# Kernel tuning notes

Measured on AMD Instinct MI355X. Metric: run time of the kernel, lower is better.

Reference implementation:

```python
import jax, jax.numpy as jnp
import numpy as np

NUM_CLASSES = 100
NUM_PROTOS = 10
FEAT_DIM = 1024
BATCH = 16384
NALL = NUM_CLASSES * NUM_PROTOS


def setup_inputs() -> dict:
    key = jax.random.key(0)
    k1, k2, k3 = jax.random.split(key, 3)
    x = jax.random.normal(k1, (BATCH, FEAT_DIM), dtype=jnp.float32)
    protos = jax.random.normal(k2, (NALL, FEAT_DIM), dtype=jnp.float32)
    enc_w = jax.random.normal(k3, (FEAT_DIM, FEAT_DIM), dtype=jnp.float32) / np.sqrt(FEAT_DIM)
    enc_b = jnp.zeros((FEAT_DIM,), dtype=jnp.float32)
    return {"x": x, "protos": protos, "enc_w": enc_w, "enc_b": enc_b}


def reference(x, protos, enc_w, enc_b):
    # encoder(protos): linear projection, (nall, F)
    ep = protos @ enc_w + enc_b
    # Pairwise euclidean distance via GEMM-based squared-distance trick:
    x_sq = jnp.sum(x * x, axis=-1, keepdims=True)            # (B, 1)
    p_sq = jnp.sum(ep * ep, axis=-1)                          # (nall,)
    d2 = x_sq - 2.0 * (x @ ep.T) + p_sq[None, :]              # (B, nall)
    d = jnp.sqrt(jnp.maximum(d2, 0.0))                        # L2 norm, clamp fp error
    # reshape matches torch: index = proto * num_classes + class
    d = d.reshape(x.shape[0], NUM_PROTOS, NUM_CLASSES)
    return jnp.min(d, axis=1)                                 # (B, num_classes)
```

## Files before the change

kernel.cpp:

```cpp
#include <hip/hip_runtime.h>
#include <hip/hip_bf16.h>
#include <stdint.h>

#define FEAT 1024
#define NALL 1000
#define NCLS 100

typedef __attribute__((ext_vector_type(8))) short short8;
typedef __attribute__((ext_vector_type(4))) float f32x4;
typedef __attribute__((ext_vector_type(4))) unsigned short us4;

__device__ __forceinline__ unsigned short f2bf(float f) {
    union { float f; uint32_t u; } v; v.f = f;
    uint32_t u = v.u;
    return (unsigned short)((u + 0x7FFFu + ((u >> 16) & 1u)) >> 16);
}

__device__ __forceinline__ void gload16(const void* g, void* l) {
    __builtin_amdgcn_global_load_lds((__attribute__((address_space(1))) void*)g,
                                     (__attribute__((address_space(3))) void*)l,
                                     16, 0, 0);
}

__global__ __launch_bounds__(256) void k_prep_all(const float* __restrict__ x,
                                                  unsigned short* __restrict__ xb,
                                                  float* __restrict__ xsq,
                                                  const float* __restrict__ p,
                                                  unsigned short* __restrict__ pb,
                                                  const float* __restrict__ w,
                                                  unsigned short* __restrict__ wt) {
    __shared__ float tile[32][33];
    int b = blockIdx.x;
    if (b < 4096) {
        int row = b * 4 + (threadIdx.x >> 6);
        int lane = threadIdx.x & 63;
        const float4* xr = (const float4*)(x + (size_t)row * FEAT);
        float s = 0.f;
#pragma unroll
        for (int i = 0; i < 4; ++i) {
            float4 v = xr[lane + i * 64];
            s += v.x * v.x + v.y * v.y + v.z * v.z + v.w * v.w;
            us4 o;
            o[0] = f2bf(v.x); o[1] = f2bf(v.y); o[2] = f2bf(v.z); o[3] = f2bf(v.w);
            *(us4*)(xb + (size_t)row * FEAT + (size_t)(lane + i * 64) * 4) = o;
        }
#pragma unroll
        for (int off = 32; off; off >>= 1) s += __shfl_xor(s, off);
        if (lane == 0) xsq[row] = s;
    } else if (b < 5120) {
        int row = b - 4096, t = threadIdx.x;
        us4 o;
        if (row < NALL) {
            float4 v = ((const float4*)(p + (size_t)row * FEAT))[t];
            o[0] = f2bf(v.x); o[1] = f2bf(v.y); o[2] = f2bf(v.z); o[3] = f2bf(v.w);
        } else {
            o[0] = 0; o[1] = 0; o[2] = 0; o[3] = 0;
        }
        *(us4*)(pb + (size_t)row * FEAT + (size_t)t * 4) = o;
    } else {
        int bb = b - 5120;
        int bx = bb & 31, by = bb >> 5;
        int tx = threadIdx.x & 31, ty = threadIdx.x >> 5;
#pragma unroll
        for (int i = 0; i < 4; ++i) {
            int r = by * 32 + ty + i * 8;
            tile[ty + i * 8][tx] = w[(size_t)r * FEAT + bx * 32 + tx];
        }
        __syncthreads();
#pragma unroll
        for (int i = 0; i < 4; ++i) {
            int r = bx * 32 + ty + i * 8;
            wt[(size_t)r * FEAT + by * 32 + tx] = f2bf(tile[tx][ty + i * 8]);
        }
    }
}

__global__ __launch_bounds__(256) void k_enc_gemm(const unsigned short* __restrict__ A,
                                                  const unsigned short* __restrict__ B,
                                                  const float* __restrict__ bias,
                                                  unsigned short* __restrict__ epb,
                                                  float* __restrict__ psq) {
    __shared__ __align__(16) char smem[16384];
    int bm0 = (blockIdx.x >> 4) * 64;
    int bn0 = (blockIdx.x & 15) * 64;
    int tid = threadIdx.x, lane = tid & 63, wid = tid >> 6;
    int wm = wid >> 1, wn = wid & 1;
    int ls = lane >> 4, lf = lane & 15;
    f32x4 acc[2][2] = {};
    for (int k0 = 0; k0 < FEAT; k0 += 64) {
        __syncthreads();
#pragma unroll
        for (int i = 0; i < 2; ++i) {
            int ci = wid + i * 4;
            int r = ci * 8 + (lane >> 3), c = (lane & 7) * 8;
            gload16(A + (size_t)(bm0 + r) * FEAT + k0 + c, smem + ci * 1024);
            gload16(B + (size_t)(bn0 + r) * FEAT + k0 + c, smem + 8192 + ci * 1024);
        }
        __syncthreads();
#pragma unroll
        for (int kk = 0; kk < 64; kk += 32) {
            short8 a[2], b[2];
#pragma unroll
            for (int f = 0; f < 2; ++f) {
                a[f] = *(const short8*)(smem + (wm * 32 + f * 16 + lf) * 128 + (kk + ls * 8) * 2);
                b[f] = *(const short8*)(smem + 8192 + (wn * 32 + f * 16 + lf) * 128 + (kk + ls * 8) * 2);
            }
#pragma unroll
            for (int fm = 0; fm < 2; ++fm)
#pragma unroll
                for (int fn = 0; fn < 2; ++fn)
                    acc[fm][fn] = __builtin_amdgcn_mfma_f32_16x16x32_bf16(a[fm], b[fn], acc[fm][fn], 0, 0, 0);
        }
    }
    int tr = ls * 4, tc = lf;
    float sq[2][4] = {};
#pragma unroll
    for (int fn = 0; fn < 2; ++fn) {
        int col = bn0 + wn * 32 + fn * 16 + tc;
        float bb = bias[col];
#pragma unroll
        for (int fm = 0; fm < 2; ++fm) {
#pragma unroll
            for (int r = 0; r < 4; ++r) {
                int row = bm0 + wm * 32 + fm * 16 + tr + r;
                if (row < NALL) {
                    unsigned short us = f2bf(acc[fm][fn][r] + bb);
                    union { uint32_t u; float f; } c; c.u = ((uint32_t)us) << 16;
                    sq[fm][r] += c.f * c.f;
                    int pr = (row % 100) * 10 + row / 100;
                    epb[(size_t)pr * FEAT + col] = us;
                }
            }
        }
    }
#pragma unroll
    for (int fm = 0; fm < 2; ++fm)
#pragma unroll
        for (int r = 0; r < 4; ++r) {
            float s = sq[fm][r];
            s += __shfl_xor(s, 1); s += __shfl_xor(s, 2);
            s += __shfl_xor(s, 4); s += __shfl_xor(s, 8);
            int row = bm0 + wm * 32 + fm * 16 + tr + r;
            if (lf == 0 && row < NALL) {
                int pr = (row % 100) * 10 + row / 100;
                atomicAdd(psq + pr, s);
            }
        }
}

__global__ __launch_bounds__(256, 4) void k_main(const unsigned short* __restrict__ xb,
                                                 const unsigned short* __restrict__ epb,
                                                 const float* __restrict__ xsq,
                                                 const float* __restrict__ psq,
                                                 float* __restrict__ out) {
    __shared__ __align__(16) char smem[27648];
    const int bid = blockIdx.x;
    const int swz = (bid & 7) * 208 + (bid >> 3);
    const int bm0 = (swz / 13) * 128;
    const int nt  = swz % 13;
    const int bn0 = (nt < 12) ? nt * 80 : 920;
    const int cls0 = (nt < 12) ? nt * 8 : 92;
    const int tid = threadIdx.x, lane = tid & 63, wid = tid >> 6;
    const int ls = lane >> 4, lf = lane & 15;
    float* xsq_s = (float*)(smem + 26624);
    float* psq_s = (float*)(smem + 27136);
    if (tid < 128) xsq_s[tid] = xsq[bm0 + tid];
    if (tid < 80)  psq_s[tid] = psq[bn0 + tid];

    const int sr = lane >> 3, scb = lane & 7;
    const int scol = ((scb ^ sr) << 3);
    const unsigned short* aptr[4];
    const unsigned short* bptr[3];
#pragma unroll
    for (int i = 0; i < 4; ++i)
        aptr[i] = xb + (size_t)(bm0 + (wid + i * 4) * 8 + sr) * FEAT + scol;
#pragma unroll
    for (int j = 0; j < 3; ++j) {
        int cj = wid + j * 4;
        bptr[j] = epb + (size_t)(bn0 + (cj < 10 ? cj : 0) * 8 + sr) * FEAT + scol;
    }

    int raA[2], raB[5];
#pragma unroll
    for (int f = 0; f < 2; ++f) raA[f] = (wid * 32 + f * 16 + lf) * 128;
#pragma unroll
    for (int f = 0; f < 5; ++f) raB[f] = 16384 + (f * 16 + lf) * 128;
    const int sw = lf & 7;

    f32x4 acc[2][5] = {};

    for (int t = 0; t < 16; ++t) {
        __syncthreads();
#pragma unroll
        for (int i = 0; i < 4; ++i)
            gload16(aptr[i], smem + (wid + i * 4) * 1024);
#pragma unroll
        for (int j = 0; j < 3; ++j) {
            int cj = wid + j * 4;
            if (cj < 10) gload16(bptr[j], smem + 16384 + cj * 1024);
        }
#pragma unroll
        for (int i = 0; i < 4; ++i) aptr[i] += 64;
#pragma unroll
        for (int j = 0; j < 3; ++j) bptr[j] += 64;
        __syncthreads();
#pragma unroll
        for (int kk2 = 0; kk2 < 2; ++kk2) {
            const int off = (((kk2 * 4 + ls) ^ sw) << 4);
            short8 a[2], b[5];
#pragma unroll
            for (int f = 0; f < 2; ++f)
                a[f] = *(const short8*)(smem + raA[f] + off);
#pragma unroll
            for (int f = 0; f < 5; ++f)
                b[f] = *(const short8*)(smem + raB[f] + off);
#pragma unroll
            for (int fm = 0; fm < 2; ++fm)
#pragma unroll
                for (int fn = 0; fn < 5; ++fn)
                    acc[fm][fn] = __builtin_amdgcn_mfma_f32_16x16x32_bf16(a[fm], b[fn], acc[fm][fn], 0, 0, 0);
        }
    }

    float* dls = (float*)smem;
    const int tr = ls * 4;
#pragma unroll
    for (int p = 0; p < 2; ++p) {
        __syncthreads();
#pragma unroll
        for (int fn = 0; fn < 5; ++fn) {
            int col = fn * 16 + lf;
            float pq = psq_s[col];
#pragma unroll
            for (int r = 0; r < 4; ++r) {
                float d2 = xsq_s[wid * 32 + p * 16 + tr + r] - 2.f * acc[p][fn][r] + pq;
                dls[(wid * 16 + tr + r) * 81 + col] = sqrtf(fmaxf(d2, 0.f));
            }
        }
        __syncthreads();
#pragma unroll
        for (int i = 0; i < 2; ++i) {
            int task = tid + i * 256;
            int rr = task >> 3, cl = task & 7;
            float m = 1e30f;
#pragma unroll
            for (int j = 0; j < 10; ++j) m = fminf(m, dls[rr * 81 + cl * 10 + j]);
            int grow = bm0 + (rr >> 4) * 32 + p * 16 + (rr & 15);
            out[(size_t)grow * NCLS + cls0 + cl] = m;
        }
    }
}

extern "C" void kernel_launch(void* const* d_in, const int* in_sizes, int n_in,
                              void* d_out, int out_size, void* d_ws, size_t ws_size,
                              hipStream_t stream) {
    const float* x      = (const float*)d_in[0];
    const float* protos = (const float*)d_in[1];
    const float* enc_w  = (const float*)d_in[2];
    const float* enc_b  = (const float*)d_in[3];
    float* out = (float*)d_out;
    char* ws = (char*)d_ws;

    unsigned short* xb  = (unsigned short*)ws;
    unsigned short* epb = (unsigned short*)(ws + 33554432);
    unsigned short* prb = (unsigned short*)(ws + 35651584);
    unsigned short* wtb = (unsigned short*)(ws + 37748736);
    float* xsq = (float*)(ws + 39845888);
    float* psq = (float*)(ws + 39911424);

    hipMemsetAsync(psq, 0, (size_t)NALL * 4, stream);

    k_prep_all<<<6144, 256, 0, stream>>>(x, xb, xsq, protos, prb, enc_w, wtb);
    k_enc_gemm<<<256, 256, 0, stream>>>(prb, wtb, enc_b, epb, psq);
    k_main<<<1664, 256, 0, stream>>>(xb, epb, xsq, psq, out);
}
```

Before: 99.29 us.

## Load A fragments directly to registers and double-buffer B tiles in LDS

Each wave now reads its A (x) MFMA fragments straight from global memory into registers, prefetching the next k-step while the current one computes. The B (prototype) tiles are double-buffered in LDS so the next tile's global_load_lds overlaps with the MFMA work, which leaves one barrier per iteration instead of two. Shared memory shrinks and the occupancy hint of 4 blocks is dropped from launch bounds. The risks are higher register pressure from the prefetch registers and less coalesced A loads, each lane fetching 16B pieces from a different row.

```diff
diff --git a/kernel.cpp b/kernel.cpp
--- a/kernel.cpp
+++ b/kernel.cpp
@@ -148,12 +148,12 @@
         }
 }
 
-__global__ __launch_bounds__(256, 4) void k_main(const unsigned short* __restrict__ xb,
-                                                 const unsigned short* __restrict__ epb,
-                                                 const float* __restrict__ xsq,
-                                                 const float* __restrict__ psq,
-                                                 float* __restrict__ out) {
-    __shared__ __align__(16) char smem[27648];
+__global__ __launch_bounds__(256) void k_main(const unsigned short* __restrict__ xb,
+                                              const unsigned short* __restrict__ epb,
+                                              const float* __restrict__ xsq,
+                                              const float* __restrict__ psq,
+                                              float* __restrict__ out) {
+    __shared__ __align__(16) char smem[22016];
     const int bid = blockIdx.x;
     const int swz = (bid & 7) * 208 + (bid >> 3);
     const int bm0 = (swz / 13) * 128;
@@ -162,64 +162,80 @@
     const int cls0 = (nt < 12) ? nt * 8 : 92;
     const int tid = threadIdx.x, lane = tid & 63, wid = tid >> 6;
     const int ls = lane >> 4, lf = lane & 15;
-    float* xsq_s = (float*)(smem + 26624);
-    float* psq_s = (float*)(smem + 27136);
+    float* xsq_s = (float*)(smem + 20992);
+    float* psq_s = (float*)(smem + 21504);
     if (tid < 128) xsq_s[tid] = xsq[bm0 + tid];
     if (tid < 80)  psq_s[tid] = psq[bn0 + tid];
 
+    const unsigned short* ga[2];
+#pragma unroll
+    for (int f = 0; f < 2; ++f)
+        ga[f] = xb + (size_t)(bm0 + wid * 32 + f * 16 + lf) * FEAT + ls * 8;
+
     const int sr = lane >> 3, scb = lane & 7;
     const int scol = ((scb ^ sr) << 3);
-    const unsigned short* aptr[4];
     const unsigned short* bptr[3];
-#pragma unroll
-    for (int i = 0; i < 4; ++i)
-        aptr[i] = xb + (size_t)(bm0 + (wid + i * 4) * 8 + sr) * FEAT + scol;
 #pragma unroll
     for (int j = 0; j < 3; ++j) {
         int cj = wid + j * 4;
         bptr[j] = epb + (size_t)(bn0 + (cj < 10 ? cj : 0) * 8 + sr) * FEAT + scol;
     }
 
-    int raA[2], raB[5];
-#pragma unroll
-    for (int f = 0; f < 2; ++f) raA[f] = (wid * 32 + f * 16 + lf) * 128;
-#pragma unroll
-    for (int f = 0; f < 5; ++f) raB[f] = 16384 + (f * 16 + lf) * 128;
+    int raB[5];
+#pragma unroll
+    for (int f = 0; f < 5; ++f) raB[f] = (f * 16 + lf) * 128;
     const int sw = lf & 7;
 
     f32x4 acc[2][5] = {};
-
+    short8 aC[2][2], aN[2][2];
+
+#pragma unroll
+    for (int f = 0; f < 2; ++f)
+#pragma unroll
+        for (int k2 = 0; k2 < 2; ++k2)
+            aC[f][k2] = *(const short8*)(ga[f] + k2 * 32);
+#pragma unroll
+    for (int j = 0; j < 3; ++j) {
+        int cj = wid + j * 4;
+        if (cj < 10) gload16(bptr[j], smem + cj * 1024);
+    }
+    __syncthreads();
+
+#pragma unroll
     for (int t = 0; t < 16; ++t) {
-        __syncthreads();
-#pragma unroll
-        for (int i = 0; i < 4; ++i)
-            gload16(aptr[i], smem + (wid + i * 4) * 1024);
-#pragma unroll
-        for (int j = 0; j < 3; ++j) {
-            int cj = wid + j * 4;
-            if (cj < 10) gload16(bptr[j], smem + 16384 + cj * 1024);
-        }
-#pragma unroll
-        for (int i = 0; i < 4; ++i) aptr[i] += 64;
-#pragma unroll
-        for (int j = 0; j < 3; ++j) bptr[j] += 64;
-        __syncthreads();
-#pragma unroll
-        for (int kk2 = 0; kk2 < 2; ++kk2) {
-            const int off = (((kk2 * 4 + ls) ^ sw) << 4);
-            short8 a[2], b[5];
+        const char* base = (const char*)smem + (t & 1) * 10240;
+        if (t < 15) {
 #pragma unroll
             for (int f = 0; f < 2; ++f)
-                a[f] = *(const short8*)(smem + raA[f] + off);
+#pragma unroll
+                for (int k2 = 0; k2 < 2; ++k2)
+                    aN[f][k2] = *(const short8*)(ga[f] + (t + 1) * 64 + k2 * 32);
+            char* nb = (char*)smem + ((t + 1) & 1) * 10240;
+#pragma unroll
+            for (int j = 0; j < 3; ++j) {
+                int cj = wid + j * 4;
+                if (cj < 10) gload16(bptr[j] + (t + 1) * 64, nb + cj * 1024);
+            }
+        }
+#pragma unroll
+        for (int k2 = 0; k2 < 2; ++k2) {
+            const int off = (((k2 * 4 + ls) ^ sw) << 4);
+            short8 b[5];
 #pragma unroll
             for (int f = 0; f < 5; ++f)
-                b[f] = *(const short8*)(smem + raB[f] + off);
+                b[f] = *(const short8*)(base + raB[f] + off);
 #pragma unroll
             for (int fm = 0; fm < 2; ++fm)
 #pragma unroll
                 for (int fn = 0; fn < 5; ++fn)
-                    acc[fm][fn] = __builtin_amdgcn_mfma_f32_16x16x32_bf16(a[fm], b[fn], acc[fm][fn], 0, 0, 0);
-        }
+                    acc[fm][fn] = __builtin_amdgcn_mfma_f32_16x16x32_bf16(aC[fm][k2], b[fn], acc[fm][fn], 0, 0, 0);
+        }
+        __syncthreads();
+#pragma unroll
+        for (int f = 0; f < 2; ++f)
+#pragma unroll
+            for (int k2 = 0; k2 < 2; ++k2)
+                aC[f][k2] = aN[f][k2];
     }
 
     float* dls = (float*)smem;
```

Measured after the change: 125.6 us. 1.26x slower.
